# Optimization experiments

Measured on AMD Instinct MI355X. Metric: run time of the kernel, lower is better.

## Reference

```python
import jax, jax.numpy as jnp
import numpy as np
from jax import lax

K_TOP = 4
NF1, NF2 = 6, 14
KS1, KS2 = 7, 5


def conv1d_grouped(x, w, b, groups, pad):
    # x: (B, Cin, L), w: (Cout, Cin//groups, K)
    y = lax.conv_general_dilated(x, w, window_strides=(1,), padding=[(pad, pad)],
                                 dimension_numbers=('NCH', 'OIH', 'NCH'),
                                 feature_group_count=groups)
    return y + b[None, :, None]


def kmax_pool(x, k):
    # order-preserving k-max along last axis
    idx = jnp.sort(lax.top_k(x, k)[1], axis=-1)
    return jnp.take_along_axis(x, idx, axis=-1)


def fold_sum(h, b, nf, rows, L):
    # h: (B, rows*nf, L) with group-major channel layout (rows groups of nf)
    h = h.reshape(b, rows, nf, L).transpose(0, 2, 1, 3)        # (B, nf, rows, L)
    h = h.reshape(b, nf, rows // 2, 2, L).sum(axis=3)          # Fold(2,2): sum adjacent row pairs
    return h.transpose(0, 2, 1, 3).reshape(b, (rows // 2) * nf, L)


def setup_inputs() -> dict:
    key = jax.random.key(0)
    ks = jax.random.split(key, 8)
    V, D, C, B, S = 50257, 256, 1000, 32, 1024
    x = jax.random.randint(ks[0], (B, S), 0, V)
    emb = jax.random.normal(ks[1], (V, D), jnp.float32)
    w1 = jax.random.normal(ks[2], (NF1 * D, 1, KS1), jnp.float32) * 0.1
    b1 = jnp.zeros((NF1 * D,), jnp.float32)
    w2 = jax.random.normal(ks[3], (NF2 * (D // 2), NF1, KS2), jnp.float32) * 0.05
    b2 = jnp.zeros((NF2 * (D // 2),), jnp.float32)
    wf = jax.random.normal(ks[4], (C, NF2 * (D // 4) * K_TOP), jnp.float32) * 0.02
    bf = jnp.zeros((C,), jnp.float32)
    return {"x": x, "emb": emb, "w1": w1, "b1": b1, "w2": w2, "b2": b2, "wf": wf, "bf": bf}


def reference(x, emb, w1, b1, w2, b2, wf, bf):
    D = emb.shape[1]
    B = x.shape[0]
    h = emb[x].transpose(0, 2, 1)                 # (B, D, S)
    h = conv1d_grouped(h, w1, b1, groups=D, pad=KS1 - 1)   # (B, 6D, S+6)
    L1 = h.shape[-1]
    h = fold_sum(h, B, NF1, D, L1)                # (B, 3D, L1)
    # dynamic k-max: layer 1 of 2 -> k = max(k_top, ceil(L/2))
    k1 = max(K_TOP, -(-L1 // 2))
    h = jnp.tanh(kmax_pool(h, k1))
    h = conv1d_grouped(h, w2, b2, groups=D // 2, pad=KS2 - 1)  # (B, 7D, k1+4)
    L2 = h.shape[-1]
    h = fold_sum(h, B, NF2, D // 2, L2)           # (B, 14*(D/4), L2)
    h = jnp.tanh(kmax_pool(h, K_TOP))             # (B, 14*(D/4), k_top)
    # dropout is identity in eval mode
    h = h.reshape(B, -1)
    return h @ wf.T + bf
```

## Files before the change

kernel.cpp:

```cpp
#include <hip/hip_runtime.h>
#include <hip/hip_bf16.h>


typedef __attribute__((ext_vector_type(8))) short short8;
typedef __attribute__((ext_vector_type(4))) float f32x4;

__device__ __forceinline__ float fast_tanh(float x) {
    float e = __expf(2.f * x);
    return 1.f - 2.f / (e + 1.f);
}

__device__ __forceinline__ unsigned fkey(float f) {
    unsigned u = __float_as_uint(f);
    return (u & 0x80000000u) ? ~u : (u | 0x80000000u);
}

__device__ __forceinline__ float fkey_inv(unsigned k) {
    unsigned u = (k & 0x80000000u) ? (k ^ 0x80000000u) : ~k;
    return __uint_as_float(u);
}

__device__ __forceinline__ unsigned short f2bf_rne(float f) {
    unsigned u = __float_as_uint(f);
    return (unsigned short)((u + 0x7fffu + ((u >> 16) & 1u)) >> 16);
}

__global__ __launch_bounds__(256) void gather_kernel(
    const int* __restrict__ x, const float* __restrict__ emb, float* __restrict__ E2)
{
    const int b = blockIdx.x >> 4;
    const int c64 = blockIdx.x & 15;
    const int wv = threadIdx.x >> 6, lane = threadIdx.x & 63;
    float* dst = E2 + ((((size_t)b << 6) + lane) << 12);
#pragma unroll
    for (int t = 0; t < 16; ++t) {
        int l = (c64 << 6) + (wv << 4) + t;
        int tok = x[(b << 10) + l];
        float4 v = *(const float4*)(emb + ((size_t)tok << 8) + (lane << 2));
        *(float4*)(dst + (size_t)l * 4) = v;
    }
}

__global__ __launch_bounds__(896) void stage12_kernel(
    const int* __restrict__ x, const float* __restrict__ emb,
    const float* __restrict__ w1, const float* __restrict__ b1,
    const float* __restrict__ w2, const float* __restrict__ b2,
    const float* __restrict__ E2,
    __hip_bfloat16* __restrict__ H)
{
    __shared__ __align__(16) float e[4 * 1104];
    __shared__ __align__(16) float F[12 * 584];
    const int b = blockIdx.x >> 6;
    const int r2 = blockIdx.x & 63;
    const int tid = threadIdx.x;

    for (int i = tid; i < 12 * 584; i += 896) F[i] = 0.f;
    if (E2) {
        const float* E2blk = E2 + ((((size_t)b << 6) + r2) << 12);
        for (int idx = tid; idx < 1104; idx += 896) {
            int l = idx - 6;
            float4 v = {0.f, 0.f, 0.f, 0.f};
            if (l >= 0 && l < 1024) v = *(const float4*)(E2blk + (size_t)l * 4);
            e[0 * 1104 + idx] = v.x; e[1 * 1104 + idx] = v.y;
            e[2 * 1104 + idx] = v.z; e[3 * 1104 + idx] = v.w;
        }
    } else {
        for (int idx = tid; idx < 1104; idx += 896) {
            int l = idx - 6;
            float4 v = {0.f, 0.f, 0.f, 0.f};
            if (l >= 0 && l < 1024) {
                int tok = x[(b << 10) + l];
                v = *(const float4*)(emb + ((size_t)tok << 8) + (r2 << 2));
            }
            e[0 * 1104 + idx] = v.x; e[1 * 1104 + idx] = v.y;
            e[2 * 1104 + idx] = v.z; e[3 * 1104 + idx] = v.w;
        }
    }
    __syncthreads();

    const int w = tid >> 6;
    const int lane = tid & 63;

    if (w < 12) {
        const int half = (w >= 6) ? 1 : 0;
        const int f = w - half * 6;
        const float* ep0 = e + (2 * half) * 1104;
        const float* ep1 = ep0 + 1104;
        const int c0 = __builtin_amdgcn_readfirstlane((2 * (2 * r2 + half)) * 6 + f);
        const int c1 = c0 + 6;
        float wA[7], wB[7];
#pragma unroll
        for (int t = 0; t < 7; ++t) { wA[t] = w1[c0 * 7 + t]; wB[t] = w1[c1 * 7 + t]; }
        const float bias = b1[c0] + b1[c1];

        const int pos0 = lane * 17;
        float a0[7], a1[7];
#pragma unroll
        for (int t = 0; t < 7; ++t) { a0[t] = ep0[pos0 + t]; a1[t] = ep1[pos0 + t]; }

        unsigned key[17];
#pragma unroll
        for (int j = 0; j < 17; ++j) {
            float a = bias;
#pragma unroll
            for (int t = 0; t < 7; ++t) a += a0[t] * wA[t] + a1[t] * wB[t];
            key[j] = (pos0 + j < 1030) ? fkey(a) : 0u;
            if (j < 16) {
#pragma unroll
                for (int t = 0; t < 6; ++t) { a0[t] = a0[t + 1]; a1[t] = a1[t + 1]; }
                a0[6] = ep0[pos0 + j + 7];
                a1[6] = ep1[pos0 + j + 7];
            }
        }

        unsigned T = 0u;
        for (int bit = 31; bit >= 0; --bit) {
            unsigned cand = T | (1u << bit);
            int cnt = 0;
#pragma unroll
            for (int j = 0; j < 17; ++j) cnt += (int)__popcll(__ballot(key[j] >= cand));
            if (cnt >= 515) T = cand;
            if (cnt == 515) break;
        }

        const unsigned long long lm = (1ull << lane) - 1ull;
        int gt_tot = 0, gt_run = 0, eq_run = 0;
#pragma unroll
        for (int j = 0; j < 17; ++j) {
            unsigned long long bg = __ballot(key[j] > T);
            unsigned long long be = __ballot(key[j] == T);
            gt_tot += (int)__popcll(bg);
            gt_run += (int)__popcll(bg & lm);
            eq_run += (int)__popcll(be & lm);
        }
        const int q = 515 - gt_tot;
        float* Frow = F + w * 584;
#pragma unroll
        for (int j = 0; j < 17; ++j) {
            bool isgt = key[j] > T;
            bool iseq = key[j] == T;
            int pos = gt_run + (eq_run < q ? eq_run : q);
            if (isgt || (iseq && eq_run < q)) Frow[4 + pos] = fast_tanh(fkey_inv(key[j]));
            gt_run += isgt ? 1 : 0;
            eq_run += iseq ? 1 : 0;
        }
    }
    __syncthreads();

    {
        const int j = w;
        const int base = lane * 9;
        const int bidx = __builtin_amdgcn_readfirstlane((2 * r2) * 14 + j);
        const float bias2 = b2[bidx] + b2[bidx + 14];
        float acc[9];
#pragma unroll
        for (int jj = 0; jj < 9; ++jj) acc[jj] = bias2;

#pragma unroll
        for (int i = 0; i < 12; ++i) {
            const float* Fr = F + i * 584 + base;
            const int cg = 2 * r2 + ((i >= 6) ? 1 : 0);
            const int ii = (i >= 6) ? (i - 6) : i;
            const int widx = __builtin_amdgcn_readfirstlane(((cg * 14 + j) * 6 + ii) * 5);
            float wv[5];
#pragma unroll
            for (int t = 0; t < 5; ++t) wv[t] = w2[widx + t];
            float win[5];
#pragma unroll
            for (int t = 0; t < 5; ++t) win[t] = Fr[t];
#pragma unroll
            for (int jj = 0; jj < 9; ++jj) {
#pragma unroll
                for (int t = 0; t < 5; ++t) acc[jj] += win[t] * wv[t];
                if (jj < 8) {
#pragma unroll
                    for (int t = 0; t < 4; ++t) win[t] = win[t + 1];
                    win[4] = Fr[jj + 5];
                }
            }
        }

        float vv[9];
#pragma unroll
        for (int jj = 0; jj < 9; ++jj) vv[jj] = (base + jj < 519) ? acc[jj] : -INFINITY;
        float sv[4]; int si[4];
#pragma unroll
        for (int it = 0; it < 4; ++it) {
            float m = vv[0]; int mi = base;
#pragma unroll
            for (int jj = 1; jj < 9; ++jj) { if (vv[jj] > m) { m = vv[jj]; mi = base + jj; } }
#pragma unroll
            for (int d = 1; d < 64; d <<= 1) {
                float om = __shfl_xor(m, d, 64);
                int omi = __shfl_xor(mi, d, 64);
                if (om > m || (om == m && omi < mi)) { m = om; mi = omi; }
            }
            sv[it] = m; si[it] = mi;
            int lj = mi - base;
#pragma unroll
            for (int jj = 0; jj < 9; ++jj) if (jj == lj) vv[jj] = -INFINITY;
        }
#define CSWAP(a, bq) { if (si[a] > si[bq]) { int ti = si[a]; si[a] = si[bq]; si[bq] = ti; \
                                             float tv = sv[a]; sv[a] = sv[bq]; sv[bq] = tv; } }
        CSWAP(0, 1) CSWAP(2, 3) CSWAP(0, 2) CSWAP(1, 3) CSWAP(1, 2)
#undef CSWAP
        if (lane == 0) {
            __hip_bfloat16* op = H + (size_t)b * 3584 + (r2 * 14 + j) * 4;
#pragma unroll
            for (int k = 0; k < 4; ++k) op[k] = __float2bfloat16(fast_tanh(sv[k]));
        }
    }
}

__global__ __launch_bounds__(256) void bias_init_kernel(
    const float* __restrict__ bfv, float* __restrict__ out)
{
    int idx = blockIdx.x * 256 + threadIdx.x;
    if (idx < 32000) out[idx] = bfv[idx - (idx / 1000) * 1000];
}

__global__ __launch_bounds__(256) void stage3_kernel(
    const __hip_bfloat16* __restrict__ Hb, const float* __restrict__ wf,
    float* __restrict__ out)
{
    __shared__ __align__(16) float sred[2 * 4 * 256];
    const int nt = blockIdx.x % 63;
    const int kc = blockIdx.x / 63;
    const int w = threadIdx.x >> 6, lane = threadIdx.x & 63;
    const int row = lane & 15, quad = lane >> 4;
    const int c = nt * 16 + row;
    const bool cvalid = (c < 1000);
    const int kofs = kc * 896 + w * 224 + quad * 8;
    const __hip_bfloat16* ap0 = Hb + (size_t)row * 3584 + kofs;
    const __hip_bfloat16* ap1 = ap0 + (size_t)16 * 3584;
    const float* bp = wf + (size_t)(cvalid ? c : 0) * 3584 + kofs;

    f32x4 acc0 = {0.f, 0.f, 0.f, 0.f};
    f32x4 acc1 = {0.f, 0.f, 0.f, 0.f};
#pragma unroll
    for (int it = 0; it < 7; ++it) {
        short8 a0 = *(const short8*)(ap0 + it * 32);
        short8 a1 = *(const short8*)(ap1 + it * 32);
        float4 p0 = *(const float4*)(bp + it * 32);
        float4 p1 = *(const float4*)(bp + it * 32 + 4);
        short8 bfr;
        bfr[0] = (short)f2bf_rne(p0.x); bfr[1] = (short)f2bf_rne(p0.y);
        bfr[2] = (short)f2bf_rne(p0.z); bfr[3] = (short)f2bf_rne(p0.w);
        bfr[4] = (short)f2bf_rne(p1.x); bfr[5] = (short)f2bf_rne(p1.y);
        bfr[6] = (short)f2bf_rne(p1.z); bfr[7] = (short)f2bf_rne(p1.w);
        if (!cvalid) bfr = short8{0, 0, 0, 0, 0, 0, 0, 0};
        acc0 = __builtin_amdgcn_mfma_f32_16x16x32_bf16(a0, bfr, acc0, 0, 0, 0);
        acc1 = __builtin_amdgcn_mfma_f32_16x16x32_bf16(a1, bfr, acc1, 0, 0, 0);
    }
#pragma unroll
    for (int r_ = 0; r_ < 4; ++r_) {
        sred[(0 * 4 + w) * 256 + lane * 4 + r_] = acc0[r_];
        sred[(1 * 4 + w) * 256 + lane * 4 + r_] = acc1[r_];
    }
    __syncthreads();
    if (threadIdx.x < 128) {
        const int mt = threadIdx.x >> 6;
        const int l2 = threadIdx.x & 63;
        const int rr = l2 & 15, qq = l2 >> 4;
        const int cc = nt * 16 + rr;
        if (cc < 1000) {
            const float* sp = sred + mt * 4 * 256;
#pragma unroll
            for (int r_ = 0; r_ < 4; ++r_) {
                float s = sp[0 * 256 + l2 * 4 + r_] + sp[1 * 256 + l2 * 4 + r_]
                        + sp[2 * 256 + l2 * 4 + r_] + sp[3 * 256 + l2 * 4 + r_];
                int brow = mt * 16 + qq * 4 + r_;
                atomicAdd(&out[brow * 1000 + cc], s);
            }
        }
    }
}

extern "C" void kernel_launch(void* const* d_in, const int* in_sizes, int n_in,
                              void* d_out, int out_size, void* d_ws, size_t ws_size,
                              hipStream_t stream) {
    const int* x      = (const int*)d_in[0];
    const float* emb  = (const float*)d_in[1];
    const float* w1   = (const float*)d_in[2];
    const float* b1   = (const float*)d_in[3];
    const float* w2   = (const float*)d_in[4];
    const float* b2   = (const float*)d_in[5];
    const float* wf   = (const float*)d_in[6];
    const float* bfv  = (const float*)d_in[7];

    const size_t E2_BYTES = (size_t)32 * 64 * 1024 * 4 * 4;
    const size_t H_BYTES  = (size_t)32 * 3584 * 2;
    float* E2 = nullptr;
    __hip_bfloat16* H;
    if (ws_size >= E2_BYTES + H_BYTES) {
        E2 = (float*)d_ws;
        H = (__hip_bfloat16*)((char*)d_ws + E2_BYTES);
    } else {
        H = (__hip_bfloat16*)d_ws;
    }

    bias_init_kernel<<<125, 256, 0, stream>>>(bfv, (float*)d_out);
    if (E2) gather_kernel<<<32 * 16, 256, 0, stream>>>(x, emb, E2);
    stage12_kernel<<<32 * 64, 896, 0, stream>>>(x, emb, w1, b1, w2, b2, E2, H);
    stage3_kernel<<<63 * 4, 256, 0, stream>>>(H, wf, (float*)d_out);
}
```

Before: 259.8 us.

## Shrink stage12 block to 640 threads, fuse bias init into gather, resplit stage3

```diff
diff --git a/kernel.cpp b/kernel.cpp
--- a/kernel.cpp
+++ b/kernel.cpp
@@ -25,9 +25,15 @@
     return (unsigned short)((u + 0x7fffu + ((u >> 16) & 1u)) >> 16);
 }
 
-__global__ __launch_bounds__(256) void gather_kernel(
-    const int* __restrict__ x, const float* __restrict__ emb, float* __restrict__ E2)
+__global__ __launch_bounds__(256) void gather_bias_kernel(
+    const int* __restrict__ x, const float* __restrict__ emb, float* __restrict__ E2,
+    const float* __restrict__ bfv, float* __restrict__ out)
 {
+    if (blockIdx.x >= 512) {
+        int idx = (blockIdx.x - 512) * 256 + threadIdx.x;
+        if (idx < 32000) out[idx] = bfv[idx - (idx / 1000) * 1000];
+        return;
+    }
     const int b = blockIdx.x >> 4;
     const int c64 = blockIdx.x & 15;
     const int wv = threadIdx.x >> 6, lane = threadIdx.x & 63;
@@ -41,7 +47,14 @@
     }
 }
 
-__global__ __launch_bounds__(896) void stage12_kernel(
+__global__ __launch_bounds__(256) void bias_init_kernel(
+    const float* __restrict__ bfv, float* __restrict__ out)
+{
+    int idx = blockIdx.x * 256 + threadIdx.x;
+    if (idx < 32000) out[idx] = bfv[idx - (idx / 1000) * 1000];
+}
+
+__global__ __launch_bounds__(640) void stage12_kernel(
     const int* __restrict__ x, const float* __restrict__ emb,
     const float* __restrict__ w1, const float* __restrict__ b1,
     const float* __restrict__ w2, const float* __restrict__ b2,
@@ -54,10 +67,10 @@
     const int r2 = blockIdx.x & 63;
     const int tid = threadIdx.x;
 
-    for (int i = tid; i < 12 * 584; i += 896) F[i] = 0.f;
+    for (int i = tid; i < 12 * 584; i += 640) F[i] = 0.f;
     if (E2) {
         const float* E2blk = E2 + ((((size_t)b << 6) + r2) << 12);
-        for (int idx = tid; idx < 1104; idx += 896) {
+        for (int idx = tid; idx < 1104; idx += 640) {
             int l = idx - 6;
             float4 v = {0.f, 0.f, 0.f, 0.f};
             if (l >= 0 && l < 1024) v = *(const float4*)(E2blk + (size_t)l * 4);
@@ -65,7 +78,7 @@
             e[2 * 1104 + idx] = v.z; e[3 * 1104 + idx] = v.w;
         }
     } else {
-        for (int idx = tid; idx < 1104; idx += 896) {
+        for (int idx = tid; idx < 1104; idx += 640) {
             int l = idx - 6;
             float4 v = {0.f, 0.f, 0.f, 0.f};
             if (l >= 0 && l < 1024) {
@@ -81,142 +94,143 @@
     const int w = tid >> 6;
     const int lane = tid & 63;
 
-    if (w < 12) {
-        const int half = (w >= 6) ? 1 : 0;
-        const int f = w - half * 6;
-        const float* ep0 = e + (2 * half) * 1104;
-        const float* ep1 = ep0 + 1104;
-        const int c0 = __builtin_amdgcn_readfirstlane((2 * (2 * r2 + half)) * 6 + f);
-        const int c1 = c0 + 6;
-        float wA[7], wB[7];
-#pragma unroll
-        for (int t = 0; t < 7; ++t) { wA[t] = w1[c0 * 7 + t]; wB[t] = w1[c1 * 7 + t]; }
-        const float bias = b1[c0] + b1[c1];
-
-        const int pos0 = lane * 17;
-        float a0[7], a1[7];
-#pragma unroll
-        for (int t = 0; t < 7; ++t) { a0[t] = ep0[pos0 + t]; a1[t] = ep1[pos0 + t]; }
-
-        unsigned key[17];
-#pragma unroll
-        for (int j = 0; j < 17; ++j) {
-            float a = bias;
-#pragma unroll
-            for (int t = 0; t < 7; ++t) a += a0[t] * wA[t] + a1[t] * wB[t];
-            key[j] = (pos0 + j < 1030) ? fkey(a) : 0u;
-            if (j < 16) {
-#pragma unroll
-                for (int t = 0; t < 6; ++t) { a0[t] = a0[t + 1]; a1[t] = a1[t + 1]; }
-                a0[6] = ep0[pos0 + j + 7];
-                a1[6] = ep1[pos0 + j + 7];
-            }
-        }
-
-        unsigned T = 0u;
-        for (int bit = 31; bit >= 0; --bit) {
-            unsigned cand = T | (1u << bit);
-            int cnt = 0;
-#pragma unroll
-            for (int j = 0; j < 17; ++j) cnt += (int)__popcll(__ballot(key[j] >= cand));
-            if (cnt >= 515) T = cand;
-            if (cnt == 515) break;
-        }
-
-        const unsigned long long lm = (1ull << lane) - 1ull;
-        int gt_tot = 0, gt_run = 0, eq_run = 0;
-#pragma unroll
-        for (int j = 0; j < 17; ++j) {
-            unsigned long long bg = __ballot(key[j] > T);
-            unsigned long long be = __ballot(key[j] == T);
-            gt_tot += (int)__popcll(bg);
-            gt_run += (int)__popcll(bg & lm);
-            eq_run += (int)__popcll(be & lm);
-        }
-        const int q = 515 - gt_tot;
-        float* Frow = F + w * 584;
-#pragma unroll
-        for (int j = 0; j < 17; ++j) {
-            bool isgt = key[j] > T;
-            bool iseq = key[j] == T;
-            int pos = gt_run + (eq_run < q ? eq_run : q);
-            if (isgt || (iseq && eq_run < q)) Frow[4 + pos] = fast_tanh(fkey_inv(key[j]));
-            gt_run += isgt ? 1 : 0;
-            eq_run += iseq ? 1 : 0;
+    for (int rep = 0; rep < 2; ++rep) {
+        const int i = w + rep * 10;
+        if (i < 12) {
+            const int half = (i >= 6) ? 1 : 0;
+            const int f = i - half * 6;
+            const float* ep0 = e + (2 * half) * 1104;
+            const float* ep1 = ep0 + 1104;
+            const int c0 = __builtin_amdgcn_readfirstlane((2 * (2 * r2 + half)) * 6 + f);
+            const int c1 = c0 + 6;
+            float wA[7], wB[7];
+#pragma unroll
+            for (int t = 0; t < 7; ++t) { wA[t] = w1[c0 * 7 + t]; wB[t] = w1[c1 * 7 + t]; }
+            const float bias = b1[c0] + b1[c1];
+
+            const int pos0 = lane * 17;
+            float a0[7], a1[7];
+#pragma unroll
+            for (int t = 0; t < 7; ++t) { a0[t] = ep0[pos0 + t]; a1[t] = ep1[pos0 + t]; }
+
+            unsigned key[17];
+#pragma unroll
+            for (int j = 0; j < 17; ++j) {
+                float a = bias;
+#pragma unroll
+                for (int t = 0; t < 7; ++t) a += a0[t] * wA[t] + a1[t] * wB[t];
+                key[j] = (pos0 + j < 1030) ? fkey(a) : 0u;
+                if (j < 16) {
+#pragma unroll
+                    for (int t = 0; t < 6; ++t) { a0[t] = a0[t + 1]; a1[t] = a1[t + 1]; }
+                    a0[6] = ep0[pos0 + j + 7];
+                    a1[6] = ep1[pos0 + j + 7];
+                }
+            }
+
+            unsigned T = 0u;
+            for (int bit = 31; bit >= 0; --bit) {
+                unsigned cand = T | (1u << bit);
+                int cnt = 0;
+#pragma unroll
+                for (int j = 0; j < 17; ++j) cnt += (int)__popcll(__ballot(key[j] >= cand));
+                if (cnt >= 515) T = cand;
+                if (cnt == 515) break;
+            }
+
+            const unsigned long long lm = (1ull << lane) - 1ull;
+            int gt_tot = 0, gt_run = 0, eq_run = 0;
+#pragma unroll
+            for (int j = 0; j < 17; ++j) {
+                unsigned long long bg = __ballot(key[j] > T);
+                unsigned long long be = __ballot(key[j] == T);
+                gt_tot += (int)__popcll(bg);
+                gt_run += (int)__popcll(bg & lm);
+                eq_run += (int)__popcll(be & lm);
+            }
+            const int q = 515 - gt_tot;
+            float* Frow = F + i * 584;
+#pragma unroll
+            for (int j = 0; j < 17; ++j) {
+                bool isgt = key[j] > T;
+                bool iseq = key[j] == T;
+                int pos = gt_run + (eq_run < q ? eq_run : q);
+                if (isgt || (iseq && eq_run < q)) Frow[4 + pos] = fkey_inv(key[j]);
+                gt_run += isgt ? 1 : 0;
+                eq_run += iseq ? 1 : 0;
+            }
         }
     }
     __syncthreads();
 
-    {
-        const int j = w;
-        const int base = lane * 9;
-        const int bidx = __builtin_amdgcn_readfirstlane((2 * r2) * 14 + j);
-        const float bias2 = b2[bidx] + b2[bidx + 14];
-        float acc[9];
-#pragma unroll
-        for (int jj = 0; jj < 9; ++jj) acc[jj] = bias2;
-
-#pragma unroll
-        for (int i = 0; i < 12; ++i) {
-            const float* Fr = F + i * 584 + base;
-            const int cg = 2 * r2 + ((i >= 6) ? 1 : 0);
-            const int ii = (i >= 6) ? (i - 6) : i;
-            const int widx = __builtin_amdgcn_readfirstlane(((cg * 14 + j) * 6 + ii) * 5);
-            float wv[5];
-#pragma unroll
-            for (int t = 0; t < 5; ++t) wv[t] = w2[widx + t];
-            float win[5];
-#pragma unroll
-            for (int t = 0; t < 5; ++t) win[t] = Fr[t];
-#pragma unroll
-            for (int jj = 0; jj < 9; ++jj) {
-#pragma unroll
-                for (int t = 0; t < 5; ++t) acc[jj] += win[t] * wv[t];
-                if (jj < 8) {
-#pragma unroll
-                    for (int t = 0; t < 4; ++t) win[t] = win[t + 1];
-                    win[4] = Fr[jj + 5];
+    for (int i = tid; i < 12 * 584; i += 640) F[i] = fast_tanh(F[i]);
+    __syncthreads();
+
+    for (int rep = 0; rep < 2; ++rep) {
+        const int j = w + rep * 10;
+        if (j < 14) {
+            const int base = lane * 9;
+            const int bidx = __builtin_amdgcn_readfirstlane((2 * r2) * 14 + j);
+            const float bias2 = b2[bidx] + b2[bidx + 14];
+            float acc[9];
+#pragma unroll
+            for (int jj = 0; jj < 9; ++jj) acc[jj] = bias2;
+
+#pragma unroll
+            for (int i = 0; i < 12; ++i) {
+                const float* Fr = F + i * 584 + base;
+                const int cg = 2 * r2 + ((i >= 6) ? 1 : 0);
+                const int ii = (i >= 6) ? (i - 6) : i;
+                const int widx = __builtin_amdgcn_readfirstlane(((cg * 14 + j) * 6 + ii) * 5);
+                float wv[5];
+#pragma unroll
+                for (int t = 0; t < 5; ++t) wv[t] = w2[widx + t];
+                float win[5];
+#pragma unroll
+                for (int t = 0; t < 5; ++t) win[t] = Fr[t];
+#pragma unroll
+                for (int jj = 0; jj < 9; ++jj) {
+#pragma unroll
+                    for (int t = 0; t < 5; ++t) acc[jj] += win[t] * wv[t];
+                    if (jj < 8) {
+#pragma unroll
+                        for (int t = 0; t < 4; ++t) win[t] = win[t + 1];
+                        win[4] = Fr[jj + 5];
+                    }
                 }
             }
-        }
-
-        float vv[9];
-#pragma unroll
-        for (int jj = 0; jj < 9; ++jj) vv[jj] = (base + jj < 519) ? acc[jj] : -INFINITY;
-        float sv[4]; int si[4];
-#pragma unroll
-        for (int it = 0; it < 4; ++it) {
-            float m = vv[0]; int mi = base;
-#pragma unroll
-            for (int jj = 1; jj < 9; ++jj) { if (vv[jj] > m) { m = vv[jj]; mi = base + jj; } }
-#pragma unroll
-            for (int d = 1; d < 64; d <<= 1) {
-                float om = __shfl_xor(m, d, 64);
-                int omi = __shfl_xor(mi, d, 64);
-                if (om > m || (om == m && omi < mi)) { m = om; mi = omi; }
-            }
-            sv[it] = m; si[it] = mi;
-            int lj = mi - base;
-#pragma unroll
-            for (int jj = 0; jj < 9; ++jj) if (jj == lj) vv[jj] = -INFINITY;
-        }
+
+            float vv[9];
+#pragma unroll
+            for (int jj = 0; jj < 9; ++jj) vv[jj] = (base + jj < 519) ? acc[jj] : -INFINITY;
+            float sv[4]; int si[4];
+#pragma unroll
+            for (int it = 0; it < 4; ++it) {
+                float m = vv[0]; int mi = base;
+#pragma unroll
+                for (int jj = 1; jj < 9; ++jj) { if (vv[jj] > m) { m = vv[jj]; mi = base + jj; } }
+#pragma unroll
+                for (int d = 1; d < 64; d <<= 1) {
+                    float om = __shfl_xor(m, d, 64);
+                    int omi = __shfl_xor(mi, d, 64);
+                    if (om > m || (om == m && omi < mi)) { m = om; mi = omi; }
+                }
+                sv[it] = m; si[it] = mi;
+                int lj = mi - base;
+#pragma unroll
+                for (int jj = 0; jj < 9; ++jj) if (jj == lj) vv[jj] = -INFINITY;
+            }
 #define CSWAP(a, bq) { if (si[a] > si[bq]) { int ti = si[a]; si[a] = si[bq]; si[bq] = ti; \
                                              float tv = sv[a]; sv[a] = sv[bq]; sv[bq] = tv; } }
-        CSWAP(0, 1) CSWAP(2, 3) CSWAP(0, 2) CSWAP(1, 3) CSWAP(1, 2)
+            CSWAP(0, 1) CSWAP(2, 3) CSWAP(0, 2) CSWAP(1, 3) CSWAP(1, 2)
 #undef CSWAP
-        if (lane == 0) {
-            __hip_bfloat16* op = H + (size_t)b * 3584 + (r2 * 14 + j) * 4;
-#pragma unroll
-            for (int k = 0; k < 4; ++k) op[k] = __float2bfloat16(fast_tanh(sv[k]));
-        }
-    }
-}
-
-__global__ __launch_bounds__(256) void bias_init_kernel(
-    const float* __restrict__ bfv, float* __restrict__ out)
-{
-    int idx = blockIdx.x * 256 + threadIdx.x;
-    if (idx < 32000) out[idx] = bfv[idx - (idx / 1000) * 1000];
+            if (lane == 0) {
+                __hip_bfloat16* op = H + (size_t)b * 3584 + (r2 * 14 + j) * 4;
+#pragma unroll
+                for (int k = 0; k < 4; ++k) op[k] = __float2bfloat16(fast_tanh(sv[k]));
+            }
+        }
+    }
 }
 
 __global__ __launch_bounds__(256) void stage3_kernel(
@@ -230,7 +244,7 @@
     const int row = lane & 15, quad = lane >> 4;
     const int c = nt * 16 + row;
     const bool cvalid = (c < 1000);
-    const int kofs = kc * 896 + w * 224 + quad * 8;
+    const int kofs = kc * 512 + w * 128 + quad * 8;
     const __hip_bfloat16* ap0 = Hb + (size_t)row * 3584 + kofs;
     const __hip_bfloat16* ap1 = ap0 + (size_t)16 * 3584;
     const float* bp = wf + (size_t)(cvalid ? c : 0) * 3584 + kofs;
@@ -238,7 +252,7 @@
     f32x4 acc0 = {0.f, 0.f, 0.f, 0.f};
     f32x4 acc1 = {0.f, 0.f, 0.f, 0.f};
 #pragma unroll
-    for (int it = 0; it < 7; ++it) {
+    for (int it = 0; it < 4; ++it) {
         short8 a0 = *(const short8*)(ap0 + it * 32);
         short8 a1 = *(const short8*)(ap1 + it * 32);
         float4 p0 = *(const float4*)(bp + it * 32);
@@ -299,8 +313,11 @@
         H = (__hip_bfloat16*)d_ws;
     }
 
-    bias_init_kernel<<<125, 256, 0, stream>>>(bfv, (float*)d_out);
-    if (E2) gather_kernel<<<32 * 16, 256, 0, stream>>>(x, emb, E2);
-    stage12_kernel<<<32 * 64, 896, 0, stream>>>(x, emb, w1, b1, w2, b2, E2, H);
-    stage3_kernel<<<63 * 4, 256, 0, stream>>>(H, wf, (float*)d_out);
-}
+    if (E2) {
+        gather_bias_kernel<<<512 + 125, 256, 0, stream>>>(x, emb, E2, bfv, (float*)d_out);
+    } else {
+        bias_init_kernel<<<125, 256, 0, stream>>>(bfv, (float*)d_out);
+    }
+    stage12_kernel<<<32 * 64, 640, 0, stream>>>(x, emb, w1, b1, w2, b2, E2, H);
+    stage3_kernel<<<63 * 7, 256, 0, stream>>>(H, wf, (float*)d_out);
+}
```

Measured after the change: 294.8 us. 1.13x slower.
